# Performance work log

Measured on AMD Instinct MI355X. Metric: run time of the kernel, lower is better.

The kernel has to match this reference:

```python
import jax, jax.numpy as jnp
import numpy as np

POOL_SIZE = 512
TOPK = 8
PRE_SEQ_LEN = 32
HIDDEN = 1024
EPS = 1e-8  # torch cosine_similarity eps


def setup_inputs() -> dict:
    key = jax.random.key(0)
    k1, k2, k3 = jax.random.split(key, 3)
    querys = jax.random.normal(k1, (1024, HIDDEN), dtype=jnp.float32)
    # learned params: keys initialized zeros in torch, but use randn so cosine is non-degenerate
    prompts_key = jax.random.normal(k2, (POOL_SIZE, HIDDEN), dtype=jnp.float32)
    prompts = jax.random.uniform(k3, (POOL_SIZE, PRE_SEQ_LEN, HIDDEN), dtype=jnp.float32)
    return {"querys": querys, "prompts_key": prompts_key, "prompts": prompts}


def reference(querys, prompts_key, prompts):
    # cosine similarity: [B, P]
    qn = querys / jnp.maximum(jnp.linalg.norm(querys, axis=-1, keepdims=True), EPS)
    kn = prompts_key / jnp.maximum(jnp.linalg.norm(prompts_key, axis=-1, keepdims=True), EPS)
    similarity = jnp.einsum('bh,ph->bp', qn, kn)
    # topk (sorted descending, like torch.topk); gathered sims equal topk values
    top_sim, indices = jax.lax.top_k(similarity, TOPK)  # [B, K], [B, K]
    gathered_prompts = jnp.take(prompts, indices, axis=0)  # [B, K, L, H]
    return gathered_prompts, top_sim
```

## Files before the change

### kernel.cpp

```cpp
#include <hip/hip_runtime.h>
#include <math.h>

#define NB 1024
#define NP 512
#define NH 1024
#define NK 8
#define NL 32
#define NBK (NB * NK)
#define SLICE (NL * NH)
#define EPSF 1e-8f

typedef float f32x4 __attribute__((ext_vector_type(4)));

__global__ __launch_bounds__(256) void norms_kernel(
    const float* __restrict__ q, const float* __restrict__ pk,
    float* __restrict__ qinv, float* __restrict__ kinv) {
  int row = blockIdx.x * 4 + (threadIdx.x >> 6);
  int lane = threadIdx.x & 63;
  const float* src;
  float* dst;
  if (row < NB) {
    src = q + (size_t)row * NH;
    dst = qinv + row;
  } else {
    int r = row - NB;
    if (r >= NP) return;
    src = pk + (size_t)r * NH;
    dst = kinv + r;
  }
  const float4* v = (const float4*)src;
  float s = 0.f;
#pragma unroll
  for (int i = 0; i < (NH / 4) / 64; ++i) {
    float4 x = v[lane + i * 64];
    s += x.x * x.x + x.y * x.y + x.z * x.z + x.w * x.w;
  }
#pragma unroll
  for (int off = 32; off; off >>= 1) s += __shfl_xor(s, off);
  if (lane == 0) *dst = 1.f / fmaxf(sqrtf(s), EPSF);
}

__global__ __launch_bounds__(256) void sim_kernel(
    const float* __restrict__ q, const float* __restrict__ pk,
    const float* __restrict__ qinv, const float* __restrict__ kinv,
    float* __restrict__ sim) {
  __shared__ float As[32][34];
  __shared__ float Bs[32][34];
  const int bm = blockIdx.x;
  const int bn = blockIdx.y;
  const int tid = threadIdx.x;
  const int tx = tid & 15;
  const int ty = tid >> 4;
  const int lrow = tid >> 3;
  const int lcol = (tid & 7) * 4;

  float acc00 = 0.f, acc01 = 0.f, acc10 = 0.f, acc11 = 0.f;

  const float* qrow = q + (size_t)(bm * 32 + lrow) * NH + lcol;
  const float* krow = pk + (size_t)(bn * 32 + lrow) * NH + lcol;

  for (int kt = 0; kt < NH; kt += 32) {
    float4 a = *(const float4*)(qrow + kt);
    float4 b = *(const float4*)(krow + kt);
    __syncthreads();
    As[lcol + 0][lrow] = a.x; As[lcol + 1][lrow] = a.y;
    As[lcol + 2][lrow] = a.z; As[lcol + 3][lrow] = a.w;
    Bs[lcol + 0][lrow] = b.x; Bs[lcol + 1][lrow] = b.y;
    Bs[lcol + 2][lrow] = b.z; Bs[lcol + 3][lrow] = b.w;
    __syncthreads();
#pragma unroll
    for (int k = 0; k < 32; ++k) {
      float2 a01 = *(const float2*)&As[k][2 * ty];
      float2 b01 = *(const float2*)&Bs[k][2 * tx];
      acc00 += a01.x * b01.x; acc01 += a01.x * b01.y;
      acc10 += a01.y * b01.x; acc11 += a01.y * b01.y;
    }
  }

  const int r0 = bm * 32 + 2 * ty;
  const int c0 = bn * 32 + 2 * tx;
  const float qi0 = qinv[r0], qi1 = qinv[r0 + 1];
  const float ki0 = kinv[c0], ki1 = kinv[c0 + 1];
  sim[(size_t)(r0 + 0) * NP + c0 + 0] = acc00 * qi0 * ki0;
  sim[(size_t)(r0 + 0) * NP + c0 + 1] = acc01 * qi0 * ki1;
  sim[(size_t)(r0 + 1) * NP + c0 + 0] = acc10 * qi1 * ki0;
  sim[(size_t)(r0 + 1) * NP + c0 + 1] = acc11 * qi1 * ki1;
}

__global__ __launch_bounds__(256) void topk_kernel(
    const float* __restrict__ sim, float* __restrict__ top_sim, int* __restrict__ top_idx) {
  int row = blockIdx.x * 4 + (threadIdx.x >> 6);
  int lane = threadIdx.x & 63;
  if (row >= NB) return;

  float vals[NP / 64];
#pragma unroll
  for (int i = 0; i < NP / 64; ++i) vals[i] = sim[(size_t)row * NP + lane + i * 64];

  for (int t = 0; t < NK; ++t) {
    float bv = vals[0];
    int bi = 0;
#pragma unroll
    for (int i = 1; i < NP / 64; ++i) {
      if (vals[i] > bv) { bv = vals[i]; bi = i; }
    }
    float v = bv;
    int p = lane + bi * 64;
#pragma unroll
    for (int off = 32; off; off >>= 1) {
      float ov = __shfl_xor(v, off);
      int op = __shfl_xor(p, off);
      if (ov > v || (ov == v && op < p)) { v = ov; p = op; }
    }
    if (lane == 0) {
      top_sim[row * NK + t] = v;
      top_idx[row * NK + t] = p;
    }
    if ((p & 63) == lane) {
      int wi = p >> 6;
#pragma unroll
      for (int i = 0; i < NP / 64; ++i)
        if (i == wi) vals[i] = -INFINITY;
    }
  }
}

__global__ __launch_bounds__(512) void sortperm_kernel(
    const int* __restrict__ idx, int* __restrict__ order) {
  __shared__ int hist[NP];
  __shared__ int offs[NP];
  const int t = threadIdx.x;
  hist[t] = 0;
  __syncthreads();
  for (int i = t; i < NBK; i += 512) atomicAdd(&hist[idx[i]], 1);
  __syncthreads();
  int sum = 0;
  for (int i = 0; i < t; ++i) sum += hist[i];
  offs[t] = sum;
  __syncthreads();
  for (int i = t; i < NBK; i += 512) {
    int p = idx[i];
    int pos = atomicAdd(&offs[p], 1);
    order[pos] = i;
  }
}

__global__ __launch_bounds__(256) void gather_sorted(
    const float* __restrict__ prompts, const int* __restrict__ idx,
    const int* __restrict__ order, float* __restrict__ out, int skip_slice) {
  const int j = order[blockIdx.x];
  if (j == skip_slice) return;
  const int p = idx[j];
  const f32x4* __restrict__ src = (const f32x4*)(prompts + (size_t)p * SLICE);
  f32x4* __restrict__ dst = (f32x4*)(out + (size_t)j * SLICE);
  const int t = threadIdx.x;
#pragma unroll
  for (int i = 0; i < (SLICE / 4) / 256; ++i) {
    f32x4 v = src[t + i * 256];
    __builtin_nontemporal_store(v, &dst[t + i * 256]);
  }
}

__global__ __launch_bounds__(256) void gather_tail(
    const float* __restrict__ prompts, const int* __restrict__ idx,
    float* __restrict__ out, int j) {
  const int p = idx[j];
  __syncthreads();
  const f32x4* __restrict__ src = (const f32x4*)(prompts + (size_t)p * SLICE);
  f32x4* __restrict__ dst = (f32x4*)(out + (size_t)j * SLICE);
  const int t = threadIdx.x;
#pragma unroll
  for (int i = 0; i < (SLICE / 4) / 256; ++i) {
    f32x4 v = src[t + i * 256];
    __builtin_nontemporal_store(v, &dst[t + i * 256]);
  }
}

extern "C" void kernel_launch(void* const* d_in, const int* in_sizes, int n_in,
                              void* d_out, int out_size, void* d_ws, size_t ws_size,
                              hipStream_t stream) {
  const float* querys = (const float*)d_in[0];
  const float* prompts_key = (const float*)d_in[1];
  const float* prompts = (const float*)d_in[2];
  float* out = (float*)d_out;

  const size_t GATHER = (size_t)NBK * SLICE;
  float* top_sim = out + GATHER;

  float* sim = out;
  float* qinv = out + (size_t)NB * NP;
  float* kinv = qinv + NB;

  int* idx;
  int* order;
  int skip_slice;
  if (ws_size >= 2 * NBK * sizeof(int)) {
    idx = (int*)d_ws;
    order = idx + NBK;
    skip_slice = -1;
  } else {
    idx = (int*)(out + (size_t)(NBK - 2) * SLICE);
    order = idx + NBK;
    skip_slice = NBK - 2;
  }

  norms_kernel<<<(NB + NP) / 4, 256, 0, stream>>>(querys, prompts_key, qinv, kinv);

  dim3 gsim(NB / 32, NP / 32);
  sim_kernel<<<gsim, 256, 0, stream>>>(querys, prompts_key, qinv, kinv, sim);

  topk_kernel<<<NB / 4, 256, 0, stream>>>(sim, top_sim, idx);

  sortperm_kernel<<<1, 512, 0, stream>>>(idx, order);

  gather_sorted<<<NBK, 256, 0, stream>>>(prompts, idx, order, out, skip_slice);

  if (skip_slice >= 0) {
    gather_tail<<<1, 256, 0, stream>>>(prompts, idx, out, skip_slice);
  }
}
```

Measured before the change: 298.9 us.

## Compute cosine similarity with split-bf16 MFMA instead of scalar FP32 GEMM

Normalizes queries and keys up front and splits each normalized value into three bf16 terms (hi/mid/lo), stored as planes in the output scratch region. The similarity GEMM then runs on bf16 16x16x32 MFMA instructions, summing six cross-term products to approach FP32 accuracy, which replaces the scalar LDS-tiled FP32 loop. The aim is to cut the cost of the similarity matmul, at the price of extra conversion work and more operand traffic. Dropping some cross terms could perturb top-k ordering for near-tied values.

```diff
diff --git a/kernel.cpp b/kernel.cpp
--- a/kernel.cpp
+++ b/kernel.cpp
@@ -11,80 +11,116 @@
 #define EPSF 1e-8f
 
 typedef float f32x4 __attribute__((ext_vector_type(4)));
-
-__global__ __launch_bounds__(256) void norms_kernel(
+typedef short s16x8 __attribute__((ext_vector_type(8)));
+typedef unsigned short u16;
+
+__device__ __forceinline__ u16 f2bf(float x) {
+  union { float f; unsigned u; } v; v.f = x;
+  unsigned r = (v.u + 0x7FFFu + ((v.u >> 16) & 1u)) >> 16;
+  return (u16)r;
+}
+__device__ __forceinline__ float bf2f(u16 b) {
+  union { unsigned u; float f; } v; v.u = ((unsigned)b) << 16;
+  return v.f;
+}
+
+__global__ __launch_bounds__(256) void convert_kernel(
     const float* __restrict__ q, const float* __restrict__ pk,
-    float* __restrict__ qinv, float* __restrict__ kinv) {
-  int row = blockIdx.x * 4 + (threadIdx.x >> 6);
-  int lane = threadIdx.x & 63;
+    u16* __restrict__ Q3, u16* __restrict__ K3) {
+  const int row = blockIdx.x;
+  const int tid = threadIdx.x;
   const float* src;
-  float* dst;
+  u16* dst;
+  int plane;
   if (row < NB) {
     src = q + (size_t)row * NH;
-    dst = qinv + row;
+    dst = Q3 + (size_t)row * NH;
+    plane = NB * NH;
   } else {
-    int r = row - NB;
-    if (r >= NP) return;
-    src = pk + (size_t)r * NH;
-    dst = kinv + r;
-  }
-  const float4* v = (const float4*)src;
-  float s = 0.f;
-#pragma unroll
-  for (int i = 0; i < (NH / 4) / 64; ++i) {
-    float4 x = v[lane + i * 64];
-    s += x.x * x.x + x.y * x.y + x.z * x.z + x.w * x.w;
-  }
+    src = pk + (size_t)(row - NB) * NH;
+    dst = K3 + (size_t)(row - NB) * NH;
+    plane = NP * NH;
+  }
+  float4 v = ((const float4*)src)[tid];
+  float s = v.x * v.x + v.y * v.y + v.z * v.z + v.w * v.w;
 #pragma unroll
   for (int off = 32; off; off >>= 1) s += __shfl_xor(s, off);
-  if (lane == 0) *dst = 1.f / fmaxf(sqrtf(s), EPSF);
-}
-
-__global__ __launch_bounds__(256) void sim_kernel(
-    const float* __restrict__ q, const float* __restrict__ pk,
-    const float* __restrict__ qinv, const float* __restrict__ kinv,
+  __shared__ float ws[4];
+  if ((tid & 63) == 0) ws[tid >> 6] = s;
+  __syncthreads();
+  float total = ws[0] + ws[1] + ws[2] + ws[3];
+  const float inv = 1.f / fmaxf(sqrtf(total), EPSF);
+
+  float x[4] = {v.x * inv, v.y * inv, v.z * inv, v.w * inv};
+  u16 t0[4], t1[4], t2[4];
+#pragma unroll
+  for (int i = 0; i < 4; ++i) {
+    float f = x[i];
+    u16 b0 = f2bf(f);        float r1 = f - bf2f(b0);
+    u16 b1 = f2bf(r1);       float r2 = r1 - bf2f(b1);
+    u16 b2 = f2bf(r2);
+    t0[i] = b0; t1[i] = b1; t2[i] = b2;
+  }
+  ushort4* d0 = (ushort4*)(dst + tid * 4);
+  ushort4* d1 = (ushort4*)(dst + plane + tid * 4);
+  ushort4* d2 = (ushort4*)(dst + 2 * plane + tid * 4);
+  *d0 = make_ushort4(t0[0], t0[1], t0[2], t0[3]);
+  *d1 = make_ushort4(t1[0], t1[1], t1[2], t1[3]);
+  *d2 = make_ushort4(t2[0], t2[1], t2[2], t2[3]);
+}
+
+__global__ __launch_bounds__(256) void sim_mfma_kernel(
+    const u16* __restrict__ Q3, const u16* __restrict__ K3,
     float* __restrict__ sim) {
-  __shared__ float As[32][34];
-  __shared__ float Bs[32][34];
   const int bm = blockIdx.x;
   const int bn = blockIdx.y;
-  const int tid = threadIdx.x;
-  const int tx = tid & 15;
-  const int ty = tid >> 4;
-  const int lrow = tid >> 3;
-  const int lcol = (tid & 7) * 4;
-
-  float acc00 = 0.f, acc01 = 0.f, acc10 = 0.f, acc11 = 0.f;
-
-  const float* qrow = q + (size_t)(bm * 32 + lrow) * NH + lcol;
-  const float* krow = pk + (size_t)(bn * 32 + lrow) * NH + lcol;
-
-  for (int kt = 0; kt < NH; kt += 32) {
-    float4 a = *(const float4*)(qrow + kt);
-    float4 b = *(const float4*)(krow + kt);
-    __syncthreads();
-    As[lcol + 0][lrow] = a.x; As[lcol + 1][lrow] = a.y;
-    As[lcol + 2][lrow] = a.z; As[lcol + 3][lrow] = a.w;
-    Bs[lcol + 0][lrow] = b.x; Bs[lcol + 1][lrow] = b.y;
-    Bs[lcol + 2][lrow] = b.z; Bs[lcol + 3][lrow] = b.w;
-    __syncthreads();
-#pragma unroll
-    for (int k = 0; k < 32; ++k) {
-      float2 a01 = *(const float2*)&As[k][2 * ty];
-      float2 b01 = *(const float2*)&Bs[k][2 * tx];
-      acc00 += a01.x * b01.x; acc01 += a01.x * b01.y;
-      acc10 += a01.y * b01.x; acc11 += a01.y * b01.y;
-    }
-  }
-
-  const int r0 = bm * 32 + 2 * ty;
-  const int c0 = bn * 32 + 2 * tx;
-  const float qi0 = qinv[r0], qi1 = qinv[r0 + 1];
-  const float ki0 = kinv[c0], ki1 = kinv[c0 + 1];
-  sim[(size_t)(r0 + 0) * NP + c0 + 0] = acc00 * qi0 * ki0;
-  sim[(size_t)(r0 + 0) * NP + c0 + 1] = acc01 * qi0 * ki1;
-  sim[(size_t)(r0 + 1) * NP + c0 + 0] = acc10 * qi1 * ki0;
-  sim[(size_t)(r0 + 1) * NP + c0 + 1] = acc11 * qi1 * ki1;
+  const int wave = threadIdx.x >> 6;
+  const int lane = threadIdx.x & 63;
+  const int r0 = bm * 32 + (wave & 1) * 16;
+  const int c0 = bn * 32 + (wave >> 1) * 16;
+  const int koff = (lane >> 4) * 8;
+
+  const u16* aB = Q3 + (size_t)(r0 + (lane & 15)) * NH + koff;
+  const u16* bB = K3 + (size_t)(c0 + (lane & 15)) * NH + koff;
+  const int QP = NB * NH, KP = NP * NH;
+
+  f32x4 acc0 = {0.f, 0.f, 0.f, 0.f};
+  f32x4 acc1 = {0.f, 0.f, 0.f, 0.f};
+
+  for (int kc = 0; kc < NH; kc += 64) {
+    s16x8 a00 = *(const s16x8*)(aB + kc);
+    s16x8 a01 = *(const s16x8*)(aB + QP + kc);
+    s16x8 a02 = *(const s16x8*)(aB + 2 * QP + kc);
+    s16x8 b00 = *(const s16x8*)(bB + kc);
+    s16x8 b01 = *(const s16x8*)(bB + KP + kc);
+    s16x8 b02 = *(const s16x8*)(bB + 2 * KP + kc);
+    s16x8 a10 = *(const s16x8*)(aB + kc + 32);
+    s16x8 a11 = *(const s16x8*)(aB + QP + kc + 32);
+    s16x8 a12 = *(const s16x8*)(aB + 2 * QP + kc + 32);
+    s16x8 b10 = *(const s16x8*)(bB + kc + 32);
+    s16x8 b11 = *(const s16x8*)(bB + KP + kc + 32);
+    s16x8 b12 = *(const s16x8*)(bB + 2 * KP + kc + 32);
+
+    acc0 = __builtin_amdgcn_mfma_f32_16x16x32_bf16(a00, b00, acc0, 0, 0, 0);
+    acc1 = __builtin_amdgcn_mfma_f32_16x16x32_bf16(a10, b10, acc1, 0, 0, 0);
+    acc0 = __builtin_amdgcn_mfma_f32_16x16x32_bf16(a00, b01, acc0, 0, 0, 0);
+    acc1 = __builtin_amdgcn_mfma_f32_16x16x32_bf16(a10, b11, acc1, 0, 0, 0);
+    acc0 = __builtin_amdgcn_mfma_f32_16x16x32_bf16(a01, b00, acc0, 0, 0, 0);
+    acc1 = __builtin_amdgcn_mfma_f32_16x16x32_bf16(a11, b10, acc1, 0, 0, 0);
+    acc0 = __builtin_amdgcn_mfma_f32_16x16x32_bf16(a01, b01, acc0, 0, 0, 0);
+    acc1 = __builtin_amdgcn_mfma_f32_16x16x32_bf16(a11, b11, acc1, 0, 0, 0);
+    acc0 = __builtin_amdgcn_mfma_f32_16x16x32_bf16(a00, b02, acc0, 0, 0, 0);
+    acc1 = __builtin_amdgcn_mfma_f32_16x16x32_bf16(a10, b12, acc1, 0, 0, 0);
+    acc0 = __builtin_amdgcn_mfma_f32_16x16x32_bf16(a02, b00, acc0, 0, 0, 0);
+    acc1 = __builtin_amdgcn_mfma_f32_16x16x32_bf16(a12, b10, acc1, 0, 0, 0);
+  }
+
+#pragma unroll
+  for (int i = 0; i < 4; ++i) {
+    int row = r0 + (lane >> 4) * 4 + i;
+    int col = c0 + (lane & 15);
+    sim[(size_t)row * NP + col] = acc0[i] + acc1[i];
+  }
 }
 
 __global__ __launch_bounds__(256) void topk_kernel(
@@ -188,8 +224,8 @@
   float* top_sim = out + GATHER;
 
   float* sim = out;
-  float* qinv = out + (size_t)NB * NP;
-  float* kinv = qinv + NB;
+  u16* Q3 = (u16*)(out + 524288);
+  u16* K3 = (u16*)(out + 2097152);
 
   int* idx;
   int* order;
@@ -204,10 +240,10 @@
     skip_slice = NBK - 2;
   }
 
-  norms_kernel<<<(NB + NP) / 4, 256, 0, stream>>>(querys, prompts_key, qinv, kinv);
+  convert_kernel<<<NB + NP, 256, 0, stream>>>(querys, prompts_key, Q3, K3);
 
   dim3 gsim(NB / 32, NP / 32);
-  sim_kernel<<<gsim, 256, 0, stream>>>(querys, prompts_key, qinv, kinv, sim);
+  sim_mfma_kernel<<<gsim, 256, 0, stream>>>(Q3, K3, sim);
 
   topk_kernel<<<NB / 4, 256, 0, stream>>>(sim, top_sim, idx);
 
```

Measured after the change: 302.3 us. Within noise of the previous version (+1.1%).
